# Kernel tuning notes

Measured on AMD Instinct MI355X. Metric: run time of the kernel, lower is better.

Reference implementation:

```python
import jax, jax.numpy as jnp
import numpy as np

N, E, G = 50000, 800000, 64
F_IN, H, R, C = 64, 64, 3, 10


def setup_inputs() -> dict:
    key = jax.random.key(0)
    ks = jax.random.split(key, 16)
    s = 0.1
    return dict(
        x=jax.random.normal(ks[0], (N, F_IN), jnp.float32),
        edge_index=jax.random.randint(ks[1], (2, E), 0, N, dtype=jnp.int32),
        edge_type=jax.random.randint(ks[2], (E,), 0, R, dtype=jnp.int32),
        graph_batch=jnp.sort(jax.random.randint(ks[3], (N,), 0, G, dtype=jnp.int32)),
        # FiLMConv params (per-relation lin: bias=False; per-relation film: bias=True)
        film_lin_W=jax.random.normal(ks[4], (R, F_IN, H), jnp.float32) * s,
        film_film_W=jax.random.normal(ks[5], (R, F_IN, 2 * H), jnp.float32) * s,
        film_film_b=jnp.zeros((R, 2 * H), jnp.float32),
        skip_W=jax.random.normal(ks[6], (F_IN, H), jnp.float32) * s,
        skip_film_W=jax.random.normal(ks[7], (F_IN, 2 * H), jnp.float32) * s,
        skip_film_b=jnp.zeros((2 * H,), jnp.float32),
        # GATConv params (heads=1, concat=True, lin bias=False, final bias=True)
        gat_W=jax.random.normal(ks[8], (F_IN, H), jnp.float32) * s,
        gat_att_src=jax.random.normal(ks[9], (H,), jnp.float32) * s,
        gat_att_dst=jax.random.normal(ks[10], (H,), jnp.float32) * s,
        gat_b=jnp.zeros((H,), jnp.float32),
        # classifier MLP
        lin_W=jax.random.normal(ks[11], (4 * H, H), jnp.float32) * s,
        lin_b=jnp.zeros((H,), jnp.float32),
        fc_W=jax.random.normal(ks[12], (H, C), jnp.float32) * s,
        fc_b=jnp.zeros((C,), jnp.float32),
    )


def _film_conv(x, edge_index, edge_type, lin_W, film_W, film_b,
               skip_W, skip_film_W, skip_film_b):
    # PyG FiLMConv, aggr='mean' per relation, act=relu.
    n, r, h = x.shape[0], lin_W.shape[0], skip_W.shape[1]
    src, dst = edge_index[0], edge_index[1]
    fs = x @ skip_film_W + skip_film_b                  # [N,2H]; split -> (beta, gamma)
    out = jax.nn.relu(fs[:, h:] * (x @ skip_W) + fs[:, :h])
    xr = jnp.einsum('nd,rdh->rnh', x, lin_W)            # [R,N,H]
    fm = jnp.einsum('nd,rdh->rnh', x, film_W) + film_b[:, None, :]  # [R,N,2H]
    beta, gamma = fm[..., :h], fm[..., h:]
    # each edge uses its own relation's lin/film params
    msg = jax.nn.relu(gamma[edge_type, dst] * xr[edge_type, src] + beta[edge_type, dst])  # [E,H]
    seg = dst * r + edge_type                            # per-(node,relation) mean
    cnt = jax.ops.segment_sum(jnp.ones_like(msg[:, 0]), seg, num_segments=n * r)
    denom = jnp.maximum(cnt[seg], 1.0)
    agg = jax.ops.segment_sum(msg / denom[:, None], dst, num_segments=n)
    return out + agg


def _gat_conv(x, edge_index, W, att_src, att_dst, b):
    # PyG GATConv, heads=1, negative_slope=0.2, add_self_loops=True.
    n = x.shape[0]
    xp = x @ W                                           # [N,H]
    loop = jnp.arange(n, dtype=edge_index.dtype)
    src = jnp.concatenate([edge_index[0], loop])
    dst = jnp.concatenate([edge_index[1], loop])
    e = jax.nn.leaky_relu((xp @ att_src)[src] + (xp @ att_dst)[dst], 0.2)  # [E+N]
    m = jax.ops.segment_max(e, dst, num_segments=n)
    alpha = jnp.exp(e - m[dst])
    denom = jax.ops.segment_sum(alpha, dst, num_segments=n)
    alpha = alpha / denom[dst]
    return jax.ops.segment_sum(alpha[:, None] * xp[src], dst, num_segments=n) + b


def reference(x, edge_index, edge_type, graph_batch,
              film_lin_W, film_film_W, film_film_b, skip_W, skip_film_W, skip_film_b,
              gat_W, gat_att_src, gat_att_dst, gat_b,
              lin_W, lin_b, fc_W, fc_b):
    out1 = jax.nn.relu(_film_conv(x, edge_index, edge_type, film_lin_W, film_film_W,
                                  film_film_b, skip_W, skip_film_W, skip_film_b))
    out2 = jax.nn.relu(_gat_conv(x, edge_index, gat_W, gat_att_src, gat_att_dst, gat_b))
    feats = jnp.concatenate([out1, out2], axis=-1)       # [N,2H]
    g = G
    cnt = jax.ops.segment_sum(jnp.ones_like(feats[:, 0]), graph_batch, num_segments=g)
    mx = jax.ops.segment_max(feats, graph_batch, num_segments=g)
    mx = jnp.where(cnt[:, None] > 0, mx, 0.0)
    mean = jax.ops.segment_sum(feats, graph_batch, num_segments=g) / jnp.maximum(cnt, 1.0)[:, None]
    pooled = jnp.concatenate([mx, mean], axis=-1)        # [G,4H]
    hidden = jax.nn.relu(pooled @ lin_W + lin_b)         # dropout = identity (eval)
    logits = hidden @ fc_W + fc_b
    return jax.nn.log_softmax(logits, axis=-1)
```

## Files before the change

### kernel.cpp

```cpp
#include <hip/hip_runtime.h>
#include <hip/hip_bf16.h>

#define NN 50000
#define EE 800000
#define GG 64
#define RR 3
#define CC 10
#define RPL 16
#define NBG 782
#define NBS 1563

typedef __attribute__((ext_vector_type(8))) short bf16x8;
typedef __attribute__((ext_vector_type(4))) float f32x4;

__device__ inline float leaky02(float x) { return x > 0.f ? x : 0.2f * x; }

__device__ inline void atomicMaxFPos(float* addr, float v) {
  atomicMax((int*)addr, __float_as_int(v));
}

__device__ inline unsigned short f2bf(float f) {
  __hip_bfloat16 b = __float2bfloat16(f);
  return *reinterpret_cast<unsigned short*>(&b);
}
__device__ inline float bf2f(unsigned short u) {
  return __uint_as_float(((unsigned int)u) << 16);
}

__global__ void wpack_k(const float* __restrict__ skip_film_W,
                        const float* __restrict__ skip_W,
                        const float* __restrict__ film_lin_W,
                        const float* __restrict__ film_film_W,
                        const float* __restrict__ gat_W,
                        const float* __restrict__ skip_film_b,
                        const float* __restrict__ film_film_b,
                        unsigned short* __restrict__ Wt,
                        float* __restrict__ bias) {
  int idx = blockIdx.x * 256 + threadIdx.x;
  if (idx >= 832 * 64 + 832) return;
  if (idx >= 832 * 64) {
    int c = idx - 832 * 64;
    float bv = 0.f;
    if (c < 128) bv = skip_film_b[c];
    else if (c >= 384 && c < 768) bv = film_film_b[c - 384];
    bias[c] = bv;
    return;
  }
  int c = idx >> 6, k = idx & 63;
  float v;
  if (c < 128)      v = skip_film_W[k * 128 + c];
  else if (c < 192) v = skip_W[k * 64 + (c - 128)];
  else if (c < 384) { int cc = c - 192, r = cc >> 6, h = cc & 63;
                      v = film_lin_W[(r * 64 + k) * 64 + h]; }
  else if (c < 768) { int cc = c - 384, r = cc >> 7, j = cc & 127;
                      v = film_film_W[(r * 64 + k) * 128 + j]; }
  else              v = gat_W[k * 64 + (c - 768)];
  Wt[idx] = f2bf(v);
}

__global__ __launch_bounds__(256) void fuse_k(const float* __restrict__ X,
    const unsigned short* __restrict__ Wt, const float* __restrict__ bias,
    const float* __restrict__ att_src, const float* __restrict__ att_dst,
    unsigned short* __restrict__ XP, unsigned short* __restrict__ XR,
    unsigned short* __restrict__ Ybg,
    unsigned short* __restrict__ S0b, float* __restrict__ as_,
    float* __restrict__ ad_,
    const int* __restrict__ ei, const int* __restrict__ et,
    int* __restrict__ fill4, int* __restrict__ sorted) {
  __shared__ __align__(16) unsigned short As[64][72];
  __shared__ __align__(16) unsigned short Bs[128][72];
  const int tid = threadIdx.x;

  if (blockIdx.x >= NBG) {
    int e = (blockIdx.x - NBG) * 512 + tid * 2;
    if (e < EE) {
      int2 s2 = *reinterpret_cast<const int2*>(ei + e);
      int2 d2 = *reinterpret_cast<const int2*>(ei + EE + e);
      int2 t2 = *reinterpret_cast<const int2*>(et + e);
      int slot = atomicAdd(&fill4[d2.x * 4 + t2.x], 1);
      if (slot < 32) sorted[d2.x * 96 + t2.x * 32 + slot] = s2.x;
      slot = atomicAdd(&fill4[d2.y * 4 + t2.y], 1);
      if (slot < 32) sorted[d2.y * 96 + t2.y * 32 + slot] = s2.y;
    }
    return;
  }

  const int row0 = blockIdx.x * 64;
  {
    int r = tid >> 2, c0 = (tid & 3) * 16;
    int gr = row0 + r;
    ushort4 o0 = {0,0,0,0}, o1 = {0,0,0,0}, o2 = {0,0,0,0}, o3 = {0,0,0,0};
    if (gr < NN) {
      const float4* p = reinterpret_cast<const float4*>(X + (size_t)gr * 64 + c0);
      float4 v0 = p[0], v1 = p[1], v2 = p[2], v3 = p[3];
      o0 = {f2bf(v0.x), f2bf(v0.y), f2bf(v0.z), f2bf(v0.w)};
      o1 = {f2bf(v1.x), f2bf(v1.y), f2bf(v1.z), f2bf(v1.w)};
      o2 = {f2bf(v2.x), f2bf(v2.y), f2bf(v2.z), f2bf(v2.w)};
      o3 = {f2bf(v3.x), f2bf(v3.y), f2bf(v3.z), f2bf(v3.w)};
    }
    *reinterpret_cast<ushort4*>(&As[r][c0])      = o0;
    *reinterpret_cast<ushort4*>(&As[r][c0 + 4])  = o1;
    *reinterpret_cast<ushort4*>(&As[r][c0 + 8])  = o2;
    *reinterpret_cast<ushort4*>(&As[r][c0 + 12]) = o3;
  }
  __syncthreads();

  const int w = tid >> 6, lane = tid & 63;
  const int m = lane & 15, q = lane >> 4;
  bf16x8 a0 = *reinterpret_cast<const bf16x8*>(&As[16 * w + m][q * 8]);
  bf16x8 a1 = *reinterpret_cast<const bf16x8*>(&As[16 * w + m][32 + q * 8]);
  const int rbase = row0 + 16 * w + q * 4;

  f32x4 t0[8], t1[4], t6[4];

  for (int tile = 0; tile < 7; tile++) {
    __syncthreads();
    int col0 = tile * 128;
    int width = (tile == 6) ? 64 : 128;
    {
      int c = tid >> 1, half = (tid & 1) * 32;
      if (c < width) {
        int gc = col0 + c;
        const uint4* p = reinterpret_cast<const uint4*>(Wt + (size_t)gc * 64 + half);
        uint4 v0 = p[0], v1 = p[1], v2 = p[2], v3 = p[3];
        *reinterpret_cast<uint4*>(&Bs[c][half])      = v0;
        *reinterpret_cast<uint4*>(&Bs[c][half + 8])  = v1;
        *reinterpret_cast<uint4*>(&Bs[c][half + 16]) = v2;
        *reinterpret_cast<uint4*>(&Bs[c][half + 24]) = v3;
      }
    }
    __syncthreads();
    #pragma unroll
    for (int ct = 0; ct < 8; ct++) {
      if (tile == 6 && ct >= 4) continue;
      bf16x8 b0 = *reinterpret_cast<const bf16x8*>(&Bs[ct * 16 + m][q * 8]);
      bf16x8 b1 = *reinterpret_cast<const bf16x8*>(&Bs[ct * 16 + m][32 + q * 8]);
      f32x4 acc = {0.f, 0.f, 0.f, 0.f};
      acc = __builtin_amdgcn_mfma_f32_16x16x32_bf16(a0, b0, acc, 0, 0, 0);
      acc = __builtin_amdgcn_mfma_f32_16x16x32_bf16(a1, b1, acc, 0, 0, 0);
      if (tile == 0) { t0[ct] = acc; continue; }
      if (tile == 1 && ct < 4) { t1[ct] = acc; continue; }
      if (tile == 6) t6[ct] = acc;
      int colm = ct * 16 + m;
      float bv = (tile >= 3 && tile <= 5) ? bias[col0 + colm] : 0.f;
      #pragma unroll
      for (int rg = 0; rg < 4; rg++) {
        int gr = rbase + rg;
        if (gr >= NN) continue;
        float v = acc[rg];
        if (tile == 1) {
          XR[(size_t)gr * 64 + (colm - 64)] = f2bf(v);
        } else if (tile == 2) {
          if (ct < 4) XR[((size_t)NN + gr) * 64 + colm]            = f2bf(v);
          else        XR[((size_t)2 * NN + gr) * 64 + (colm - 64)] = f2bf(v);
        } else if (tile <= 5) {
          Ybg[(size_t)gr * 384 + (col0 - 384) + colm] = f2bf(v + bv);
        } else {
          XP[(size_t)gr * 64 + colm] = f2bf(v);
        }
      }
    }
  }

  float pa[4] = {0.f, 0.f, 0.f, 0.f}, pd[4] = {0.f, 0.f, 0.f, 0.f};
  #pragma unroll
  for (int j = 0; j < 4; j++) {
    int h = 16 * j + m;
    float bb = bias[h];
    float bg = bias[64 + h];
    float asv = att_src[h];
    float adv = att_dst[h];
    #pragma unroll
    for (int rg = 0; rg < 4; rg++) {
      float so = fmaxf((t0[4 + j][rg] + bg) * t1[j][rg] + (t0[j][rg] + bb), 0.f);
      int gr = rbase + rg;
      if (gr < NN) S0b[(size_t)gr * 64 + h] = f2bf(so);
      pa[rg] += t6[j][rg] * asv;
      pd[rg] += t6[j][rg] * adv;
    }
  }
  #pragma unroll
  for (int ofs = 1; ofs < 16; ofs <<= 1) {
    #pragma unroll
    for (int rg = 0; rg < 4; rg++) {
      pa[rg] += __shfl_xor(pa[rg], ofs);
      pd[rg] += __shfl_xor(pd[rg], ofs);
    }
  }
  if (m == 0) {
    #pragma unroll
    for (int rg = 0; rg < 4; rg++) {
      int gr = rbase + rg;
      if (gr < NN) { as_[gr] = pa[rg]; ad_[gr] = pd[rg]; }
    }
  }
}

#define RPN 16

__global__ __launch_bounds__(256) void dst_k(const int* __restrict__ sorted,
    const int* __restrict__ fill4, const unsigned short* __restrict__ XP,
    const unsigned short* __restrict__ XR,
    const unsigned short* __restrict__ Ybg,
    const unsigned short* __restrict__ S0b,
    const float* __restrict__ as_, const float* __restrict__ ad_,
    const float* __restrict__ gat_b, const int* __restrict__ gb,
    float* __restrict__ pmax, float* __restrict__ psum,
    int* __restrict__ gstart, int* __restrict__ gend) {
  __shared__ int   s_pk[4][96];
  __shared__ float s_w [4][96];
  __shared__ int   s_d [4][4];
  __shared__ int   s_g[4];
  __shared__ float s_ad[4];
  __shared__ __align__(16) unsigned short s_rows[64][128];
  float* s_val = (float*)&s_rows[0][0];

  const int tid = threadIdx.x;
  const int wid = tid >> 6, h = tid & 63;
  const int n0 = blockIdx.x * 4;
  const int n  = n0 + wid;

  size_t rep = (size_t)(blockIdx.x & (RPL - 1)) * GG * 128;
  pmax += rep; psum += rep;

  if (tid < 16) {
    int wd = tid >> 2, t = tid & 3;
    if (t < 3) {
      int d = fill4[(n0 + wd) * 4 + t];
      s_d[wd][t] = d > 32 ? 32 : d;
    } else {
      s_g[wd]  = gb[n0 + wd];
      s_ad[wd] = ad_[n0 + wd];
    }
  }
  __syncthreads();

  for (int i = tid; i < 512; i += 256) {
    int wd = i >> 7, s = i & 127;
    if (s < 96) {
      int tt = s >> 5, j = s & 31;
      if (j < s_d[wd][tt]) {
        int cidx = (tt == 0) ? j
                 : (tt == 1) ? s_d[wd][0] + j
                             : s_d[wd][0] + s_d[wd][1] + j;
        int src = sorted[(size_t)(n0 + wd) * 96 + s];
        s_pk[wd][cidx] = src;
        s_w[wd][cidx]  = leaky02(as_[src] + s_ad[wd]);
      }
    }
  }
  __syncthreads();

  const int d0 = s_d[wid][0], d1 = s_d[wid][1], d2 = s_d[wid][2];
  const int sB = d0 + d1;
  const int deg = sB + d2;
  const float adn = s_ad[wid];
  float es = leaky02(as_[n] + adn);

  bool v1 = h < deg;
  bool v2 = h + 64 < deg;
  float e1 = v1 ? s_w[wid][h]      : -1e30f;
  float e2 = v2 ? s_w[wid][64 + h] : -1e30f;
  float mg = fmaxf(fmaxf(e1, e2), es);
  #pragma unroll
  for (int ofs = 1; ofs < 64; ofs <<= 1) mg = fmaxf(mg, __shfl_xor(mg, ofs));
  float w1 = v1 ? __expf(e1 - mg) : 0.f;
  float w2 = v2 ? __expf(e2 - mg) : 0.f;
  if (v1) s_w[wid][h] = w1;
  if (v2) s_w[wid][64 + h] = w2;
  float den = w1 + w2;
  #pragma unroll
  for (int ofs = 1; ofs < 64; ofs <<= 1) den += __shfl_xor(den, ofs);
  float ws = __expf(es - mg);
  den += ws;

  const float i0 = 1.f / (float)(d0 > 1 ? d0 : 1);
  const float i1 = 1.f / (float)(d1 > 1 ? d1 : 1);
  const float i2 = 1.f / (float)(d2 > 1 ? d2 : 1);
  const unsigned short* ybg = Ybg + (size_t)n * 384;
  const float b0p = bf2f(ybg[h])       * i0, g0p = bf2f(ybg[64 + h])  * i0;
  const float b1p = bf2f(ybg[128 + h]) * i1, g1p = bf2f(ybg[192 + h]) * i1;
  const float b2p = bf2f(ybg[256 + h]) * i2, g2p = bf2f(ybg[320 + h]) * i2;

  float S = ws * bf2f(XP[(size_t)n * 64 + h]);
  float f = 0.f;

  const int grp16 = tid >> 4, lane16 = tid & 15;
  int kA[4], kB[4], kD[4];
  #pragma unroll
  for (int k = 0; k < 4; k++) {
    kA[k] = s_d[k][0];
    kB[k] = kA[k] + s_d[k][1];
    kD[k] = kB[k] + s_d[k][2];
  }
  int dmax = max(max(kD[0], kD[1]), max(kD[2], kD[3]));
  int rounds = (dmax + RPN - 1) / RPN;

  for (int r = 0; r < rounds; r++) {
    int e0 = r * RPN;
    #pragma unroll
    for (int k = 0; k < 4; k++) {
      int jj = e0 + grp16;
      if (jj < kD[k]) {
        int src = s_pk[k][jj];
        int t = jj < kA[k] ? 0 : (jj < kB[k] ? 1 : 2);
        const unsigned short* row = (lane16 < 8)
            ? XP + (size_t)src * 64 + lane16 * 8
            : XR + ((size_t)t * NN + src) * 64 + (lane16 - 8) * 8;
        uint4 v = *reinterpret_cast<const uint4*>(row);
        *reinterpret_cast<uint4*>(&s_rows[16 * k + grp16][lane16 * 8]) = v;
      }
    }
    __syncthreads();
    const unsigned short* rowp = &s_rows[wid * RPN][0];
    int hi0 = min(e0 + RPN, d0);
    for (int i = e0; i < hi0; i++) {
      float wj = s_w[wid][i];
      int sr = i - e0;
      float xp = bf2f(rowp[sr * 128 + h]);
      float xr = bf2f(rowp[sr * 128 + 64 + h]);
      S += wj * xp;
      f += fmaxf(g0p * xr + b0p, 0.f);
    }
    int lo1 = max(e0, d0), hi1 = min(e0 + RPN, sB);
    for (int i = lo1; i < hi1; i++) {
      float wj = s_w[wid][i];
      int sr = i - e0;
      float xp = bf2f(rowp[sr * 128 + h]);
      float xr = bf2f(rowp[sr * 128 + 64 + h]);
      S += wj * xp;
      f += fmaxf(g1p * xr + b1p, 0.f);
    }
    int lo2 = max(e0, sB), hi2 = min(e0 + RPN, deg);
    for (int i = lo2; i < hi2; i++) {
      float wj = s_w[wid][i];
      int sr = i - e0;
      float xp = bf2f(rowp[sr * 128 + h]);
      float xr = bf2f(rowp[sr * 128 + 64 + h]);
      S += wj * xp;
      f += fmaxf(g2p * xr + b2p, 0.f);
    }
    __syncthreads();
  }

  float o1 = fmaxf(bf2f(S0b[(size_t)n * 64 + h]) + f, 0.f);
  float o2 = fmaxf(S / den + gat_b[h], 0.f);

  s_val[wid * 128 + h]      = o1;
  s_val[wid * 128 + 64 + h] = o2;
  if (h == 0) {
    int g = s_g[wid];
    if (n == 0 || gb[n - 1] != g)      gstart[g] = n;
    if (n == NN - 1 || gb[n + 1] != g) gend[g] = n;
  }
  __syncthreads();
  if (tid < 128) {
    int fch = tid;
    int curg = s_g[0];
    float v0 = s_val[fch];
    float mx = v0, sm = v0;
    #pragma unroll
    for (int j = 1; j < 4; j++) {
      float v = s_val[j * 128 + fch];
      if (s_g[j] == curg) { mx = fmaxf(mx, v); sm += v; }
      else {
        atomicMaxFPos(&pmax[curg * 128 + fch], mx);
        atomicAdd(&psum[curg * 128 + fch], sm);
        curg = s_g[j]; mx = v; sm = v;
      }
    }
    atomicMaxFPos(&pmax[curg * 128 + fch], mx);
    atomicAdd(&psum[curg * 128 + fch], sm);
  }
}

__global__ __launch_bounds__(64) void head_k(const float* __restrict__ pmax,
    const float* __restrict__ psum, const int* __restrict__ gstart,
    const int* __restrict__ gend,
    const float* __restrict__ lin_W, const float* __restrict__ lin_b,
    const float* __restrict__ fc_W, const float* __restrict__ fc_b,
    float* __restrict__ out) {
  __shared__ float p[256];
  __shared__ float hid[64];
  __shared__ float lg[CC];
  __shared__ float lse;
  int g = blockIdx.x, t = threadIdx.x;
  int s = gstart[g], e = gend[g];
  int cnt = (s <= e && s < NN && s >= 0) ? (e - s + 1) : 0;
  float invc = 1.f / (float)(cnt > 1 ? cnt : 1);
  for (int i = t; i < 256; i += 64) {
    if (i < 128) {
      float mx = 0.f;
      for (int r = 0; r < RPL; r++)
        mx = fmaxf(mx, pmax[((size_t)r * GG + g) * 128 + i]);
      p[i] = mx;
    } else {
      int f = i - 128;
      float sm = 0.f;
      for (int r = 0; r < RPL; r++)
        sm += psum[((size_t)r * GG + g) * 128 + f];
      p[i] = sm * invc;
    }
  }
  __syncthreads();
  float acc = lin_b[t];
  for (int k = 0; k < 256; k++) acc += p[k] * lin_W[k * 64 + t];
  hid[t] = fmaxf(acc, 0.f);
  __syncthreads();
  if (t < CC) {
    float a = fc_b[t];
    for (int k = 0; k < 64; k++) a += hid[k] * fc_W[k * CC + t];
    lg[t] = a;
  }
  __syncthreads();
  if (t == 0) {
    float mx = lg[0];
    for (int i = 1; i < CC; i++) mx = fmaxf(mx, lg[i]);
    float sum = 0.f;
    for (int i = 0; i < CC; i++) sum += expf(lg[i] - mx);
    lse = mx + logf(sum);
  }
  __syncthreads();
  if (t < CC) out[g * CC + t] = lg[t] - lse;
}

extern "C" void kernel_launch(void* const* d_in, const int* in_sizes, int n_in,
                              void* d_out, int out_size, void* d_ws, size_t ws_size,
                              hipStream_t stream) {
  const float* x            = (const float*)d_in[0];
  const int*   edge_index   = (const int*)d_in[1];
  const int*   edge_type    = (const int*)d_in[2];
  const int*   graph_batch  = (const int*)d_in[3];
  const float* film_lin_W   = (const float*)d_in[4];
  const float* film_film_W  = (const float*)d_in[5];
  const float* film_film_b  = (const float*)d_in[6];
  const float* skip_W       = (const float*)d_in[7];
  const float* skip_film_W  = (const float*)d_in[8];
  const float* skip_film_b  = (const float*)d_in[9];
  const float* gat_W        = (const float*)d_in[10];
  const float* att_src      = (const float*)d_in[11];
  const float* att_dst      = (const float*)d_in[12];
  const float* gat_b        = (const float*)d_in[13];
  const float* lin_W        = (const float*)d_in[14];
  const float* lin_b        = (const float*)d_in[15];
  const float* fc_W         = (const float*)d_in[16];
  const float* fc_b         = (const float*)d_in[17];
  float* out                = (float*)d_out;

  float* ws = (float*)d_ws;
  const size_t N = NN, G = GG;
  size_t oXP     = 0;
  size_t oXR     = N * 32;
  size_t oYbg    = oXR + N * 96;
  size_t oS0     = oYbg + N * 192;
  size_t oAs     = oS0 + N * 32;
  size_t oAd     = oAs + N;
  size_t oWt     = oAd + N;
  size_t oBias   = oWt + 832 * 32;
  size_t oPmax   = oBias + 832;
  size_t oPsum   = oPmax + (size_t)RPL * G * 128;
  size_t oGend   = oPsum + (size_t)RPL * G * 128;
  size_t oFill   = oGend + G;
  size_t oGstart = oFill + N * 4;
  size_t oSorted = oGstart + G;

  unsigned short* XP  = (unsigned short*)(ws + oXP);
  unsigned short* XR  = (unsigned short*)(ws + oXR);
  unsigned short* Ybg = (unsigned short*)(ws + oYbg);
  unsigned short* S0b = (unsigned short*)(ws + oS0);
  float* as_    = ws + oAs;
  float* ad_    = ws + oAd;
  unsigned short* Wt  = (unsigned short*)(ws + oWt);
  float* bias   = ws + oBias;
  float* pmax   = ws + oPmax;
  float* psum   = ws + oPsum;
  int*   gend   = (int*)(ws + oGend);
  int*   fill4  = (int*)(ws + oFill);
  int*   gstart = (int*)(ws + oGstart);
  int*   sorted = (int*)(ws + oSorted);

  size_t zeroFloats = oGstart - oPmax;
  hipMemsetAsync(pmax, 0, zeroFloats * sizeof(float), stream);

  wpack_k<<<212, 256, 0, stream>>>(skip_film_W, skip_W, film_lin_W,
                                   film_film_W, gat_W, skip_film_b,
                                   film_film_b, Wt, bias);
  fuse_k<<<NBG + NBS, 256, 0, stream>>>(x, Wt, bias, att_src, att_dst,
                                        XP, XR, Ybg, S0b, as_, ad_,
                                        edge_index, edge_type, fill4, sorted);
  dst_k<<<NN / 4, 256, 0, stream>>>(sorted, fill4, XP, XR, Ybg, S0b, as_, ad_,
                                    gat_b, graph_batch, pmax, psum,
                                    gstart, gend);
  head_k<<<GG, 64, 0, stream>>>(pmax, psum, gstart, gend,
                                lin_W, lin_b, fc_W, fc_b, out);
}
```

Baseline: 239.5 us.

## Double-buffer neighbor row gathers via direct global-to-LDS loads; fold memset into pack kernel

The dst kernel's gather loop now uses two LDS buffers filled by global_load_lds instructions. Each wave loads its own node's neighbor rows one round ahead of the compute, so gather latency overlaps the accumulation. The hipMemsetAsync is replaced by a zeroing loop inside wpack_k, and fuse_k interleaves GEMM and edge-bucketing blocks (one in three) to balance the two kinds of work across the GPU. The changes add LDS use, which may cut occupancy, and rely on the direct-to-LDS load layout lining up with the row indexing.

```diff
diff --git a/kernel.cpp b/kernel.cpp
--- a/kernel.cpp
+++ b/kernel.cpp
@@ -27,6 +27,12 @@
   return __uint_as_float(((unsigned int)u) << 16);
 }
 
+__device__ inline void gl_lds16(const void* g, void* l) {
+  __builtin_amdgcn_global_load_lds(
+      (const __attribute__((address_space(1))) unsigned int*)g,
+      (__attribute__((address_space(3))) unsigned int*)l, 16, 0, 0);
+}
+
 __global__ void wpack_k(const float* __restrict__ skip_film_W,
                         const float* __restrict__ skip_W,
                         const float* __restrict__ film_lin_W,
@@ -35,8 +41,13 @@
                         const float* __restrict__ skip_film_b,
                         const float* __restrict__ film_film_b,
                         unsigned short* __restrict__ Wt,
-                        float* __restrict__ bias) {
-  int idx = blockIdx.x * 256 + threadIdx.x;
+                        float* __restrict__ bias,
+                        float* __restrict__ zbase, int zN4) {
+  int tid0 = blockIdx.x * 256 + threadIdx.x;
+  float4 z4 = {0.f, 0.f, 0.f, 0.f};
+  for (int i = tid0; i < zN4; i += gridDim.x * 256)
+    reinterpret_cast<float4*>(zbase)[i] = z4;
+  int idx = tid0;
   if (idx >= 832 * 64 + 832) return;
   if (idx >= 832 * 64) {
     int c = idx - 832 * 64;
@@ -70,9 +81,11 @@
   __shared__ __align__(16) unsigned short As[64][72];
   __shared__ __align__(16) unsigned short Bs[128][72];
   const int tid = threadIdx.x;
-
-  if (blockIdx.x >= NBG) {
-    int e = (blockIdx.x - NBG) * 512 + tid * 2;
+  const int bid = blockIdx.x;
+
+  if (bid % 3 != 0) {
+    int sb = bid - bid / 3 - 1;
+    int e = sb * 512 + tid * 2;
     if (e < EE) {
       int2 s2 = *reinterpret_cast<const int2*>(ei + e);
       int2 d2 = *reinterpret_cast<const int2*>(ei + EE + e);
@@ -85,7 +98,7 @@
     return;
   }
 
-  const int row0 = blockIdx.x * 64;
+  const int row0 = (bid / 3) * 64;
   {
     int r = tid >> 2, c0 = (tid & 3) * 16;
     int gr = row0 + r;
@@ -212,8 +225,8 @@
   __shared__ int   s_d [4][4];
   __shared__ int   s_g[4];
   __shared__ float s_ad[4];
-  __shared__ __align__(16) unsigned short s_rows[64][128];
-  float* s_val = (float*)&s_rows[0][0];
+  __shared__ __align__(16) unsigned short s_rows[2][64][128];
+  float* s_val = (float*)&s_rows[0][0][0];
 
   const int tid = threadIdx.x;
   const int wid = tid >> 6, h = tid & 63;
@@ -285,62 +298,73 @@
   float S = ws * bf2f(XP[(size_t)n * 64 + h]);
   float f = 0.f;
 
-  const int grp16 = tid >> 4, lane16 = tid & 15;
-  int kA[4], kB[4], kD[4];
+  const int lane16 = h & 15, rquad = h >> 4;
+  __syncthreads();
+
+  int dmax = deg;
   #pragma unroll
   for (int k = 0; k < 4; k++) {
-    kA[k] = s_d[k][0];
-    kB[k] = kA[k] + s_d[k][1];
-    kD[k] = kB[k] + s_d[k][2];
-  }
-  int dmax = max(max(kD[0], kD[1]), max(kD[2], kD[3]));
+    int dk = s_d[k][0] + s_d[k][1] + s_d[k][2];
+    dmax = dmax > dk ? dmax : dk;
+  }
   int rounds = (dmax + RPN - 1) / RPN;
 
-  for (int r = 0; r < rounds; r++) {
-    int e0 = r * RPN;
+  auto GLOADL = [&](int buf, int e0) {
+    int degc = deg > 0 ? deg - 1 : 0;
     #pragma unroll
-    for (int k = 0; k < 4; k++) {
-      int jj = e0 + grp16;
-      if (jj < kD[k]) {
-        int src = s_pk[k][jj];
-        int t = jj < kA[k] ? 0 : (jj < kB[k] ? 1 : 2);
-        const unsigned short* row = (lane16 < 8)
+    for (int i = 0; i < 4; i++) {
+      if (e0 + 4 * i < deg) {
+        int jj = e0 + 4 * i + rquad;
+        int jjc = jj < deg ? jj : degc;
+        int src = s_pk[wid][jjc];
+        src = (unsigned)src < NN ? src : 0;
+        int t = jjc < d0 ? 0 : (jjc < sB ? 1 : 2);
+        const unsigned short* g = (lane16 < 8)
             ? XP + (size_t)src * 64 + lane16 * 8
             : XR + ((size_t)t * NN + src) * 64 + (lane16 - 8) * 8;
-        uint4 v = *reinterpret_cast<const uint4*>(row);
-        *reinterpret_cast<uint4*>(&s_rows[16 * k + grp16][lane16 * 8]) = v;
-      }
-    }
+        gl_lds16(g, &s_rows[buf][16 * wid + 4 * i][0]);
+      }
+    }
+  };
+
+  int cur = 0;
+  if (rounds > 0) {
+    GLOADL(0, 0);
     __syncthreads();
-    const unsigned short* rowp = &s_rows[wid * RPN][0];
-    int hi0 = min(e0 + RPN, d0);
-    for (int i = e0; i < hi0; i++) {
-      float wj = s_w[wid][i];
-      int sr = i - e0;
-      float xp = bf2f(rowp[sr * 128 + h]);
-      float xr = bf2f(rowp[sr * 128 + 64 + h]);
-      S += wj * xp;
-      f += fmaxf(g0p * xr + b0p, 0.f);
-    }
-    int lo1 = max(e0, d0), hi1 = min(e0 + RPN, sB);
-    for (int i = lo1; i < hi1; i++) {
-      float wj = s_w[wid][i];
-      int sr = i - e0;
-      float xp = bf2f(rowp[sr * 128 + h]);
-      float xr = bf2f(rowp[sr * 128 + 64 + h]);
-      S += wj * xp;
-      f += fmaxf(g1p * xr + b1p, 0.f);
-    }
-    int lo2 = max(e0, sB), hi2 = min(e0 + RPN, deg);
-    for (int i = lo2; i < hi2; i++) {
-      float wj = s_w[wid][i];
-      int sr = i - e0;
-      float xp = bf2f(rowp[sr * 128 + h]);
-      float xr = bf2f(rowp[sr * 128 + 64 + h]);
-      S += wj * xp;
-      f += fmaxf(g2p * xr + b2p, 0.f);
-    }
-    __syncthreads();
+    for (int r = 0; r < rounds; r++) {
+      int e0 = r * RPN;
+      if (r + 1 < rounds) GLOADL(cur ^ 1, e0 + RPN);
+      const unsigned short* rowp = &s_rows[cur][wid * RPN][0];
+      int hi0 = min(e0 + RPN, d0);
+      for (int i = e0; i < hi0; i++) {
+        float wj = s_w[wid][i];
+        int sr = i - e0;
+        float xp = bf2f(rowp[sr * 128 + h]);
+        float xr = bf2f(rowp[sr * 128 + 64 + h]);
+        S += wj * xp;
+        f += fmaxf(g0p * xr + b0p, 0.f);
+      }
+      int lo1 = max(e0, d0), hi1 = min(e0 + RPN, sB);
+      for (int i = lo1; i < hi1; i++) {
+        float wj = s_w[wid][i];
+        int sr = i - e0;
+        float xp = bf2f(rowp[sr * 128 + h]);
+        float xr = bf2f(rowp[sr * 128 + 64 + h]);
+        S += wj * xp;
+        f += fmaxf(g1p * xr + b1p, 0.f);
+      }
+      int lo2 = max(e0, sB), hi2 = min(e0 + RPN, deg);
+      for (int i = lo2; i < hi2; i++) {
+        float wj = s_w[wid][i];
+        int sr = i - e0;
+        float xp = bf2f(rowp[sr * 128 + h]);
+        float xr = bf2f(rowp[sr * 128 + 64 + h]);
+        S += wj * xp;
+        f += fmaxf(g2p * xr + b2p, 0.f);
+      }
+      __syncthreads();
+      cur ^= 1;
+    }
   }
 
   float o1 = fmaxf(bf2f(S0b[(size_t)n * 64 + h]) + f, 0.f);
@@ -479,12 +503,11 @@
   int*   gstart = (int*)(ws + oGstart);
   int*   sorted = (int*)(ws + oSorted);
 
-  size_t zeroFloats = oGstart - oPmax;
-  hipMemsetAsync(pmax, 0, zeroFloats * sizeof(float), stream);
+  int zN4 = (int)((oGstart - oPmax) / 4);
 
   wpack_k<<<212, 256, 0, stream>>>(skip_film_W, skip_W, film_lin_W,
                                    film_film_W, gat_W, skip_film_b,
-                                   film_film_b, Wt, bias);
+                                   film_film_b, Wt, bias, pmax, zN4);
   fuse_k<<<NBG + NBS, 256, 0, stream>>>(x, Wt, bias, att_src, att_dst,
                                         XP, XR, Ybg, S0b, as_, ad_,
                                         edge_index, edge_type, fill4, sorted);
```

New measurement: 270.9 us. +13.1%, slower.

## Two-pass bucketed edge scatter with block-local coarse binning and in-kernel zeroing

Applied to the files above, without the earlier changes.

Edge bucketing is split into two passes. First, edges are coarsely binned by destination block (512 nodes) using shared-memory counters and one global atomic per bucket per block, and packed into a single int. Then a new sortb_k kernel scatters each bucket into the per-(dst,type) slots, which keeps fill4 atomics localized. Also moves the hipMemset into wpack_k and interleaves GEMM and scatter blocks (one GEMM per three blocks). This adds a kernel launch and an extra pass over the edges, and it caps each bucket at a fixed size.

```diff
diff --git a/kernel.cpp b/kernel.cpp
--- a/kernel.cpp
+++ b/kernel.cpp
@@ -9,6 +9,8 @@
 #define RPL 16
 #define NBG 782
 #define NBS 1563
+#define NCB 98
+#define CAPC 10240
 
 typedef __attribute__((ext_vector_type(8))) short bf16x8;
 typedef __attribute__((ext_vector_type(4))) float f32x4;
@@ -35,8 +37,13 @@
                         const float* __restrict__ skip_film_b,
                         const float* __restrict__ film_film_b,
                         unsigned short* __restrict__ Wt,
-                        float* __restrict__ bias) {
-  int idx = blockIdx.x * 256 + threadIdx.x;
+                        float* __restrict__ bias,
+                        float* __restrict__ zbase, int zN4) {
+  int tid0 = blockIdx.x * 256 + threadIdx.x;
+  float4 z4 = {0.f, 0.f, 0.f, 0.f};
+  for (int i = tid0; i < zN4; i += gridDim.x * 256)
+    reinterpret_cast<float4*>(zbase)[i] = z4;
+  int idx = tid0;
   if (idx >= 832 * 64 + 832) return;
   if (idx >= 832 * 64) {
     int c = idx - 832 * 64;
@@ -66,26 +73,47 @@
     unsigned short* __restrict__ S0b, float* __restrict__ as_,
     float* __restrict__ ad_,
     const int* __restrict__ ei, const int* __restrict__ et,
-    int* __restrict__ fill4, int* __restrict__ sorted) {
+    int* __restrict__ cbfill, int* __restrict__ cbuf) {
   __shared__ __align__(16) unsigned short As[64][72];
   __shared__ __align__(16) unsigned short Bs[128][72];
   const int tid = threadIdx.x;
-
-  if (blockIdx.x >= NBG) {
-    int e = (blockIdx.x - NBG) * 512 + tid * 2;
-    if (e < EE) {
-      int2 s2 = *reinterpret_cast<const int2*>(ei + e);
-      int2 d2 = *reinterpret_cast<const int2*>(ei + EE + e);
-      int2 t2 = *reinterpret_cast<const int2*>(et + e);
-      int slot = atomicAdd(&fill4[d2.x * 4 + t2.x], 1);
-      if (slot < 32) sorted[d2.x * 96 + t2.x * 32 + slot] = s2.x;
-      slot = atomicAdd(&fill4[d2.y * 4 + t2.y], 1);
-      if (slot < 32) sorted[d2.y * 96 + t2.y * 32 + slot] = s2.y;
+  const int bid = blockIdx.x;
+
+  if (bid % 3 != 0) {
+    int* s_cnt  = (int*)&As[0][0];
+    int* s_base = s_cnt + 128;
+    for (int i = tid; i < NCB; i += 256) s_cnt[i] = 0;
+    __syncthreads();
+    int sb = bid - bid / 3 - 1;
+    int e = sb * 512 + tid * 2;
+    bool val = (e < EE);
+    int2 s2 = {0, 0}, d2 = {0, 0}, t2 = {0, 0};
+    int cb0 = 0, cb1 = 0, r0 = 0, r1 = 0;
+    if (val) {
+      s2 = *reinterpret_cast<const int2*>(ei + e);
+      d2 = *reinterpret_cast<const int2*>(ei + EE + e);
+      t2 = *reinterpret_cast<const int2*>(et + e);
+      cb0 = d2.x >> 9;  r0 = atomicAdd(&s_cnt[cb0], 1);
+      cb1 = d2.y >> 9;  r1 = atomicAdd(&s_cnt[cb1], 1);
+    }
+    __syncthreads();
+    for (int i = tid; i < NCB; i += 256) {
+      int c = s_cnt[i];
+      s_base[i] = c ? atomicAdd(&cbfill[i], c) : 0;
+    }
+    __syncthreads();
+    if (val) {
+      int p0 = s_base[cb0] + r0;
+      if (p0 < CAPC)
+        cbuf[cb0 * CAPC + p0] = s2.x | (t2.x << 16) | ((d2.x & 511) << 18);
+      int p1 = s_base[cb1] + r1;
+      if (p1 < CAPC)
+        cbuf[cb1 * CAPC + p1] = s2.y | (t2.y << 16) | ((d2.y & 511) << 18);
     }
     return;
   }
 
-  const int row0 = blockIdx.x * 64;
+  const int row0 = (bid / 3) * 64;
   {
     int r = tid >> 2, c0 = (tid & 3) * 16;
     int gr = row0 + r;
@@ -196,6 +224,19 @@
   }
 }
 
+__global__ __launch_bounds__(256) void sortb_k(const int* __restrict__ cbfill,
+    const int* __restrict__ cbuf, int* __restrict__ fill4,
+    int* __restrict__ sorted) {
+  int b = blockIdx.x >> 2, qq = blockIdx.x & 3;
+  int cnt = cbfill[b]; if (cnt > CAPC) cnt = CAPC;
+  for (int i = qq * 256 + threadIdx.x; i < cnt; i += 1024) {
+    int v = cbuf[(size_t)b * CAPC + i];
+    int src = v & 0xFFFF, t = (v >> 16) & 3, dst = (b << 9) + (v >> 18);
+    int slot = atomicAdd(&fill4[dst * 4 + t], 1);
+    if (slot < 32) sorted[dst * 96 + t * 32 + slot] = src;
+  }
+}
+
 #define RPN 16
 
 __global__ __launch_bounds__(256) void dst_k(const int* __restrict__ sorted,
@@ -461,8 +502,10 @@
   size_t oPsum   = oPmax + (size_t)RPL * G * 128;
   size_t oGend   = oPsum + (size_t)RPL * G * 128;
   size_t oFill   = oGend + G;
-  size_t oGstart = oFill + N * 4;
-  size_t oSorted = oGstart + G;
+  size_t oCbf    = oFill + N * 4;
+  size_t oGstart = oCbf + 128;
+  size_t oCbuf   = oGstart + G;
+  size_t oSorted = oCbuf + (size_t)NCB * CAPC;
 
   unsigned short* XP  = (unsigned short*)(ws + oXP);
   unsigned short* XR  = (unsigned short*)(ws + oXR);
@@ -476,18 +519,20 @@
   float* psum   = ws + oPsum;
   int*   gend   = (int*)(ws + oGend);
   int*   fill4  = (int*)(ws + oFill);
+  int*   cbfill = (int*)(ws + oCbf);
   int*   gstart = (int*)(ws + oGstart);
+  int*   cbuf   = (int*)(ws + oCbuf);
   int*   sorted = (int*)(ws + oSorted);
 
-  size_t zeroFloats = oGstart - oPmax;
-  hipMemsetAsync(pmax, 0, zeroFloats * sizeof(float), stream);
+  int zN4 = (int)((oGstart - oPmax) / 4);
 
   wpack_k<<<212, 256, 0, stream>>>(skip_film_W, skip_W, film_lin_W,
                                    film_film_W, gat_W, skip_film_b,
-                                   film_film_b, Wt, bias);
+                                   film_film_b, Wt, bias, pmax, zN4);
   fuse_k<<<NBG + NBS, 256, 0, stream>>>(x, Wt, bias, att_src, att_dst,
                                         XP, XR, Ybg, S0b, as_, ad_,
-                                        edge_index, edge_type, fill4, sorted);
+                                        edge_index, edge_type, cbfill, cbuf);
+  sortb_k<<<NCB * 4, 256, 0, stream>>>(cbfill, cbuf, fill4, sorted);
   dst_k<<<NN / 4, 256, 0, stream>>>(sorted, fill4, XP, XR, Ybg, S0b, as_, ad_,
                                     gat_b, graph_batch, pmax, psum,
                                     gstart, gend);
```

After: 347.9 us. 1.45x slower.
